# Performance work log

Measured on AMD Instinct MI355X. Metric: run time of the kernel, lower is better.

Reference implementation:

```python
import jax, jax.numpy as jnp
import numpy as np

B = 8192          # batch
NS = 2048         # no_of_states -> state width = 2*NS = 4096
NH = 1024         # no_of_heads  -> action width and output width
HID = 512         # hidden_size (fixed in module)
INPUT = NS * 2 + 4 + NH   # 5124, context_input width


def _layer(key, fan_in, fan_out):
    # matches torch nn.Linear default init: U(-1/sqrt(fan_in), 1/sqrt(fan_in))
    kw, kb = jax.random.split(key)
    bound = 1.0 / np.sqrt(fan_in)
    W = jax.random.uniform(kw, (fan_in, fan_out), minval=-bound, maxval=bound, dtype=jnp.float32)
    b = jax.random.uniform(kb, (fan_out,), minval=-bound, maxval=bound, dtype=jnp.float32)
    return W, b


def setup_inputs() -> dict:
    key = jax.random.key(0)
    keys = jax.random.split(key, 20)
    inp = {
        'state': jax.random.normal(keys[0], (B, NS * 2), dtype=jnp.float32),
        'action': jax.random.normal(keys[1], (B, NH), dtype=jnp.float32),
        'task_indicator': jax.random.normal(keys[2], (B, 4), dtype=jnp.float32),
    }
    specs = [
        ('cx1_1', 4, HID * 2), ('cx1_2', HID * 2, HID * 2),
        ('cx2_1', 4, HID * 2), ('cx2_2', HID * 2, HID * 2),
        ('cx3_1', 4, HID),     ('cx3_2', HID, HID),
        ('cx4_1', 4, NH),      ('cx4_2', NH, NH),
        ('l1', INPUT, HID * 4),
        ('l2', HID * 4 + INPUT, HID * 2),
        ('l3', HID * 2 + INPUT, HID * 2),
        ('l4', HID * 2 + INPUT, HID),
        ('l5', HID, NH),
    ]
    for i, (name, fi, fo) in enumerate(specs):
        W, b = _layer(keys[3 + i], fi, fo)
        inp['W_' + name] = W
        inp['b_' + name] = b
    return inp


def _kwta(x, k_winners):
    # Faithful to the original: top-k values are scattered back to their own
    # indices and non-top-k entries are left untouched -> identity map.
    return x


def reference(state, action, task_indicator,
              W_cx1_1, b_cx1_1, W_cx1_2, b_cx1_2,
              W_cx2_1, b_cx2_1, W_cx2_2, b_cx2_2,
              W_cx3_1, b_cx3_1, W_cx3_2, b_cx3_2,
              W_cx4_1, b_cx4_1, W_cx4_2, b_cx4_2,
              W_l1, b_l1, W_l2, b_l2, W_l3, b_l3, W_l4, b_l4, W_l5, b_l5):
    ctx = jnp.concatenate([state, task_indicator, action], axis=1)  # [B, INPUT]

    # context (k-winner-count) branches; mathematically dead wrt output
    cx1 = jnp.tanh(task_indicator @ W_cx1_1 + b_cx1_1) @ W_cx1_2 + b_cx1_2
    cx2 = jnp.tanh(task_indicator @ W_cx2_1 + b_cx2_1) @ W_cx2_2 + b_cx2_2
    cx3 = jnp.tanh(task_indicator @ W_cx3_1 + b_cx3_1) @ W_cx3_2 + b_cx3_2
    cx4 = jnp.tanh(task_indicator @ W_cx4_1 + b_cx4_1) @ W_cx4_2 + b_cx4_2

    x = ctx @ W_l1 + b_l1                       # [B, 2048]
    x = _kwta(x, cx1)
    x = jnp.concatenate([x, ctx], axis=1)       # [B, 2048+INPUT]
    x = x @ W_l2 + b_l2                         # [B, 1024]
    x = _kwta(x, cx2)
    x = jnp.concatenate([x, ctx], axis=1)
    x = x @ W_l3 + b_l3                         # [B, 1024]
    x = _kwta(x, cx3)
    x = jnp.concatenate([x, ctx], axis=1)
    x = x @ W_l4 + b_l4                         # [B, 512]
    x = _kwta(x, cx4)
    out = x @ W_l5 + b_l5                       # [B, NH]
    return out
```

## Files before the change

### kernel.cpp

```cpp
#include <hip/hip_runtime.h>
#include <hip/hip_bf16.h>
#include <stdint.h>

#define B_ROWS   8192
#define CTX_REAL 5124
#define CTX_PAD  5184

typedef unsigned short u16;
typedef __attribute__((ext_vector_type(8))) short short8;
typedef __attribute__((ext_vector_type(16))) float f32x16;

#define AS1 __attribute__((address_space(1)))
#define AS3 __attribute__((address_space(3)))

__device__ __forceinline__ u16 f2bf(float f) {
    union { float f; uint32_t u; } v; v.f = f;
    uint32_t u = v.u;
    uint32_t r = 0x7fffu + ((u >> 16) & 1u);
    return (u16)((u + r) >> 16);
}

__global__ void build_ctx(const float* __restrict__ state,
                          const float* __restrict__ ti,
                          const float* __restrict__ action,
                          u16* __restrict__ ctx) {
    const int row = blockIdx.y;
    const int c2  = blockIdx.x * blockDim.x + threadIdx.x;
    const int col = c2 * 2;
    if (col >= CTX_PAD) return;

    float v0, v1;
    {
        int c = col;
        v0 = (c < 4096) ? state[(size_t)row * 4096 + c]
           : (c < 4100) ? ti[(size_t)row * 4 + (c - 4096)]
           : (c < 5124) ? action[(size_t)row * 1024 + (c - 4100)]
           : 0.0f;
        c = col + 1;
        v1 = (c < 4096) ? state[(size_t)row * 4096 + c]
           : (c < 4100) ? ti[(size_t)row * 4 + (c - 4096)]
           : (c < 5124) ? action[(size_t)row * 1024 + (c - 4100)]
           : 0.0f;
    }
    uint32_t packed = (uint32_t)f2bf(v0) | ((uint32_t)f2bf(v1) << 16);
    *(uint32_t*)&ctx[(size_t)row * CTX_PAD + col] = packed;
}

__global__ void wconv(const float* __restrict__ W, u16* __restrict__ Wt,
                      int K_real, int Kpad, int N) {
    __shared__ float tile[64][65];
    const int k0 = blockIdx.x * 64;
    const int n0 = blockIdx.y * 64;
    const int t  = threadIdx.x;
#pragma unroll
    for (int i = 0; i < 16; ++i) {
        int idx = i * 256 + t;
        int r = idx >> 6, c = idx & 63;
        int k = k0 + r;
        tile[r][c] = (k < K_real) ? W[(size_t)k * N + n0 + c] : 0.0f;
    }
    __syncthreads();
#pragma unroll
    for (int i = 0; i < 16; ++i) {
        int idx = i * 256 + t;
        int rn = idx >> 6, ck = idx & 63;
        Wt[(size_t)(n0 + rn) * Kpad + k0 + ck] = f2bf(tile[ck][rn]);
    }
}

template <int TM, int TN, int MW, int NW, bool OUT_BF16>
__global__ __launch_bounds__(256, 2)
void gemm_bias(const u16* __restrict__ A1, int lda1, int K1,
               const u16* __restrict__ A2, int lda2,
               const u16* __restrict__ Bt, int ldb, int Ktot,
               const float* __restrict__ bias,
               void* __restrict__ Cout, int ldc) {
    constexpr int FI = TM / MW / 32;
    constexpr int FJ = TN / NW / 32;
    __shared__ u16 tA[2][TM * 64];
    __shared__ u16 tB[2][TN * 64];

    const int t    = threadIdx.x;
    const int wave = t >> 6;
    const int lane = t & 63;
    const int l32  = lane & 31;
    const int half = lane >> 5;
    const int lswz = lane & 7;
    const int wr   = (wave / NW) * (TM / MW);
    const int wc   = (wave % NW) * (TN / NW);
    const int rowBase = blockIdx.x * TM;
    const int colBase = blockIdx.y * TN;

    const int srow = t >> 3;
    const int scol = ((t & 7) ^ (srow & 7)) * 8;

    const u16* gA1 = A1 + (size_t)(rowBase + srow) * lda1 + scol;
    const u16* gA2 = A2 ? (A2 + (size_t)(rowBase + srow) * lda2 + scol) : gA1;
    const u16* gB  = Bt + (size_t)(colBase + srow) * ldb + scol;

    f32x16 acc[FI][FJ] = {};

    const int nKt = Ktot >> 6;

    auto stage = [&](int kt, int buf) {
        const int k0 = kt << 6;
        const u16* srcA;
        int strideA;
        if (k0 < K1) { srcA = gA1 + k0;        strideA = lda1; }
        else         { srcA = gA2 + (k0 - K1); strideA = lda2; }
        const u16* srcB = gB + k0;
        char* ldsA = (char*)tA[buf] + wave * 1024;
        char* ldsB = (char*)tB[buf] + wave * 1024;
#pragma unroll
        for (int it = 0; it < TM / 32; ++it)
            __builtin_amdgcn_global_load_lds(
                (AS1 const void*)(srcA + (size_t)(it * 32) * strideA),
                (AS3 void*)(ldsA + it * 4096), 16, 0, 0);
#pragma unroll
        for (int it = 0; it < TN / 32; ++it)
            __builtin_amdgcn_global_load_lds(
                (AS1 const void*)(srcB + (size_t)(it * 32) * ldb),
                (AS3 void*)(ldsB + it * 4096), 16, 0, 0);
    };

    stage(0, 0);
    __syncthreads();

    for (int kt = 0; kt < nKt; ++kt) {
        const int buf = kt & 1;
        if (kt + 1 < nKt) stage(kt + 1, buf ^ 1);

        const u16* tAw = tA[buf] + wr * 64;
        const u16* tBw = tB[buf] + wc * 64;
#pragma unroll
        for (int ks = 0; ks < 4; ++ks) {
            const int kchunk = ks * 2 + half;
            const int swz    = (kchunk ^ lswz) * 8;
            short8 a[FI], b[FJ];
#pragma unroll
            for (int i = 0; i < FI; ++i)
                a[i] = *(const short8*)(tAw + (i * 32 + l32) * 64 + swz);
#pragma unroll
            for (int j = 0; j < FJ; ++j)
                b[j] = *(const short8*)(tBw + (j * 32 + l32) * 64 + swz);
#pragma unroll
            for (int i = 0; i < FI; ++i)
#pragma unroll
                for (int j = 0; j < FJ; ++j)
                    acc[i][j] = __builtin_amdgcn_mfma_f32_32x32x16_bf16(
                        a[i], b[j], acc[i][j], 0, 0, 0);
        }
        __syncthreads();
    }

    if (OUT_BF16) {
        u16* C = (u16*)Cout;
#pragma unroll
        for (int i = 0; i < FI; ++i) {
            const int rbase = rowBase + wr + i * 32 + 4 * half;
#pragma unroll
            for (int j = 0; j < FJ; ++j) {
                const int c = colBase + wc + j * 32 + l32;
                const float bb = bias[c];
#pragma unroll
                for (int reg = 0; reg < 16; ++reg) {
                    const int r = rbase + (reg & 3) + 8 * (reg >> 2);
                    C[(size_t)r * ldc + c] = f2bf(acc[i][j][reg] + bb);
                }
            }
        }
    } else {
        float* C = (float*)Cout;
#pragma unroll
        for (int i = 0; i < FI; ++i) {
            const int rbase = rowBase + wr + i * 32 + 4 * half;
#pragma unroll
            for (int j = 0; j < FJ; ++j) {
                const int c = colBase + wc + j * 32 + l32;
                const float bb = bias[c];
#pragma unroll
                for (int reg = 0; reg < 16; ++reg) {
                    const int r = rbase + (reg & 3) + 8 * (reg >> 2);
                    C[(size_t)r * ldc + c] = acc[i][j][reg] + bb;
                }
            }
        }
    }
}

extern "C" void kernel_launch(void* const* d_in, const int* in_sizes, int n_in,
                              void* d_out, int out_size, void* d_ws, size_t ws_size,
                              hipStream_t stream) {
    const float* state  = (const float*)d_in[0];
    const float* action = (const float*)d_in[1];
    const float* ti     = (const float*)d_in[2];
    const float* W_l1 = (const float*)d_in[19]; const float* b_l1 = (const float*)d_in[20];
    const float* W_l2 = (const float*)d_in[21]; const float* b_l2 = (const float*)d_in[22];
    const float* W_l3 = (const float*)d_in[23]; const float* b_l3 = (const float*)d_in[24];
    const float* W_l4 = (const float*)d_in[25]; const float* b_l4 = (const float*)d_in[26];
    const float* W_l5 = (const float*)d_in[27]; const float* b_l5 = (const float*)d_in[28];

    char* ws = (char*)d_ws;
    size_t off = 0;
    auto alloc = [&](size_t bytes) -> void* {
        void* p = ws + off;
        off += (bytes + 255) & ~(size_t)255;
        return p;
    };
    u16* ctx = (u16*)alloc((size_t)B_ROWS * CTX_PAD * 2);
    u16* x1  = (u16*)alloc((size_t)B_ROWS * 2048 * 2);
    u16* x2  = (u16*)alloc((size_t)B_ROWS * 1024 * 2);
    u16* x3  = (u16*)alloc((size_t)B_ROWS * 1024 * 2);
    u16* x4  = (u16*)alloc((size_t)B_ROWS * 512 * 2);
    u16* W1t = (u16*)alloc((size_t)2048 * 5184 * 2);
    u16* W2t = (u16*)alloc((size_t)1024 * 7232 * 2);
    u16* W3t = (u16*)alloc((size_t)1024 * 6208 * 2);
    u16* W4t = (u16*)alloc((size_t)512  * 6208 * 2);
    u16* W5t = (u16*)alloc((size_t)1024 * 512  * 2);

    build_ctx<<<dim3((CTX_PAD / 2 + 255) / 256, B_ROWS), 256, 0, stream>>>(state, ti, action, ctx);
    wconv<<<dim3(81, 32),  256, 0, stream>>>(W_l1, W1t, 5124, 5184, 2048);
    wconv<<<dim3(113, 16), 256, 0, stream>>>(W_l2, W2t, 7172, 7232, 1024);
    wconv<<<dim3(97, 16),  256, 0, stream>>>(W_l3, W3t, 6148, 6208, 1024);
    wconv<<<dim3(97, 8),   256, 0, stream>>>(W_l4, W4t, 6148, 6208, 512);
    wconv<<<dim3(8, 16),   256, 0, stream>>>(W_l5, W5t, 512, 512, 1024);

    gemm_bias<128, 128, 2, 2, true><<<dim3(64, 16), 256, 0, stream>>>(
        ctx, CTX_PAD, CTX_PAD, nullptr, 0, W1t, 5184, 5184, b_l1, x1, 2048);
    gemm_bias<128, 128, 2, 2, true><<<dim3(64, 8), 256, 0, stream>>>(
        x1, 2048, 2048, ctx, CTX_PAD, W2t, 7232, 7232, b_l2, x2, 1024);
    gemm_bias<128, 128, 2, 2, true><<<dim3(64, 8), 256, 0, stream>>>(
        x2, 1024, 1024, ctx, CTX_PAD, W3t, 6208, 6208, b_l3, x3, 1024);
    gemm_bias<128, 128, 2, 2, true><<<dim3(64, 4), 256, 0, stream>>>(
        x3, 1024, 1024, ctx, CTX_PAD, W4t, 6208, 6208, b_l4, x4, 512);
    gemm_bias<128, 128, 2, 2, false><<<dim3(64, 8), 256, 0, stream>>>(
        x4, 512, 512, nullptr, 0, W5t, 512, 512, b_l5, d_out, 1024);
}
```

Before: 956.5 us.

## Add 8-wave GEMM kernel with larger tiles and double-buffered direct-to-LDS loads

Adds a new 512-thread GEMM kernel that uses 256x256 or 256x128 block tiles, double-buffered LDS staging via global_load_lds with explicit vmcnt waits, and MFMA priority raising. Layers 1, 2, 3 and 5 switch to it, while layer 4 stays on the old kernel. The aim is to raise data reuse per block and overlap global loads with MFMA work. The trade-off is fewer blocks (256 per launch), higher register and LDS pressure, and extra barriers inside the k-loop.

Result: slower. 1.061 ms (+10.9%).

```diff
diff --git a/kernel.cpp b/kernel.cpp
--- a/kernel.cpp
+++ b/kernel.cpp
@@ -151,6 +151,141 @@
                         a[i], b[j], acc[i][j], 0, 0, 0);
         }
         __syncthreads();
+    }
+
+    if (OUT_BF16) {
+        u16* C = (u16*)Cout;
+#pragma unroll
+        for (int i = 0; i < FI; ++i) {
+            const int rbase = rowBase + wr + i * 32 + 4 * half;
+#pragma unroll
+            for (int j = 0; j < FJ; ++j) {
+                const int c = colBase + wc + j * 32 + l32;
+                const float bb = bias[c];
+#pragma unroll
+                for (int reg = 0; reg < 16; ++reg) {
+                    const int r = rbase + (reg & 3) + 8 * (reg >> 2);
+                    C[(size_t)r * ldc + c] = f2bf(acc[i][j][reg] + bb);
+                }
+            }
+        }
+    } else {
+        float* C = (float*)Cout;
+#pragma unroll
+        for (int i = 0; i < FI; ++i) {
+            const int rbase = rowBase + wr + i * 32 + 4 * half;
+#pragma unroll
+            for (int j = 0; j < FJ; ++j) {
+                const int c = colBase + wc + j * 32 + l32;
+                const float bb = bias[c];
+#pragma unroll
+                for (int reg = 0; reg < 16; ++reg) {
+                    const int r = rbase + (reg & 3) + 8 * (reg >> 2);
+                    C[(size_t)r * ldc + c] = acc[i][j][reg] + bb;
+                }
+            }
+        }
+    }
+}
+
+template <int BM, int BN, bool OUT_BF16>
+__global__ __launch_bounds__(512, 2)
+void gemm8(const u16* __restrict__ A1, int lda1, int K1,
+           const u16* __restrict__ A2, int lda2,
+           const u16* __restrict__ Bt, int ldb, int Ktot,
+           const float* __restrict__ bias,
+           void* __restrict__ Cout, int ldc) {
+    constexpr int FI  = BM / 64;
+    constexpr int FJ  = BN / 128;
+    constexpr int LPA = BM / 64;
+    constexpr int LPB = BN / 64;
+    constexpr int LPT = LPA + LPB;
+    static_assert(LPT == 8 || LPT == 6, "vmcnt literal dispatch");
+
+    __shared__ u16 tA[2][BM * 64];
+    __shared__ u16 tB[2][BN * 64];
+
+    const int t    = threadIdx.x;
+    const int wave = t >> 6;
+    const int lane = t & 63;
+    const int l32  = lane & 31;
+    const int half = lane >> 5;
+    const int lswz = lane & 7;
+    const int wr   = (wave >> 2) * (BM / 2);
+    const int wc   = (wave & 3) * (BN / 4);
+    const int rowBase = blockIdx.x * BM;
+    const int colBase = blockIdx.y * BN;
+
+    const int srow = t >> 3;
+    const int scol = ((t & 7) ^ (srow & 7)) * 8;
+
+    const u16* gA1 = A1 + (size_t)(rowBase + srow) * lda1 + scol;
+    const u16* gA2 = A2 ? (A2 + (size_t)(rowBase + srow) * lda2 + scol) : gA1;
+    const u16* gB  = Bt + (size_t)(colBase + srow) * ldb + scol;
+
+    auto stage = [&](int kt, int buf) {
+        const int k0 = kt << 6;
+        const u16* srcA;
+        int strideA;
+        if (k0 < K1) { srcA = gA1 + k0;        strideA = lda1; }
+        else         { srcA = gA2 + (k0 - K1); strideA = lda2; }
+        const u16* srcB = gB + k0;
+        char* ldsA = (char*)tA[buf] + wave * 1024;
+        char* ldsB = (char*)tB[buf] + wave * 1024;
+#pragma unroll
+        for (int it = 0; it < LPA; ++it)
+            __builtin_amdgcn_global_load_lds(
+                (AS1 const void*)(srcA + (size_t)(it * 64) * strideA),
+                (AS3 void*)(ldsA + it * 8192), 16, 0, 0);
+#pragma unroll
+        for (int it = 0; it < LPB; ++it)
+            __builtin_amdgcn_global_load_lds(
+                (AS1 const void*)(srcB + (size_t)(it * 64) * ldb),
+                (AS3 void*)(ldsB + it * 8192), 16, 0, 0);
+    };
+
+    f32x16 acc[FI][FJ] = {};
+
+    const int nKt = Ktot >> 6;
+    stage(0, 0);
+    if (nKt > 1) stage(1, 1);
+
+    for (int kt = 0; kt < nKt; ++kt) {
+        const int buf = kt & 1;
+        if (kt == nKt - 1) {
+            asm volatile("s_waitcnt vmcnt(0)" ::: "memory");
+        } else if constexpr (LPT == 8) {
+            asm volatile("s_waitcnt vmcnt(8)" ::: "memory");
+        } else {
+            asm volatile("s_waitcnt vmcnt(6)" ::: "memory");
+        }
+        __builtin_amdgcn_s_barrier();
+
+        const u16* tAw = tA[buf] + wr * 64;
+        const u16* tBw = tB[buf] + wc * 64;
+#pragma unroll
+        for (int ks = 0; ks < 4; ++ks) {
+            const int kchunk = ks * 2 + half;
+            const int swz    = (kchunk ^ lswz) * 8;
+            short8 a[FI], b[FJ];
+#pragma unroll
+            for (int i = 0; i < FI; ++i)
+                a[i] = *(const short8*)(tAw + (i * 32 + l32) * 64 + swz);
+#pragma unroll
+            for (int j = 0; j < FJ; ++j)
+                b[j] = *(const short8*)(tBw + (j * 32 + l32) * 64 + swz);
+            __builtin_amdgcn_s_setprio(1);
+#pragma unroll
+            for (int i = 0; i < FI; ++i)
+#pragma unroll
+                for (int j = 0; j < FJ; ++j)
+                    acc[i][j] = __builtin_amdgcn_mfma_f32_32x32x16_bf16(
+                        a[i], b[j], acc[i][j], 0, 0, 0);
+            __builtin_amdgcn_s_setprio(0);
+            __builtin_amdgcn_s_barrier();
+        }
+
+        if (kt + 2 < nKt) stage(kt + 2, buf);
     }
 
     if (OUT_BF16) {
@@ -225,14 +360,14 @@
     wconv<<<dim3(97, 8),   256, 0, stream>>>(W_l4, W4t, 6148, 6208, 512);
     wconv<<<dim3(8, 16),   256, 0, stream>>>(W_l5, W5t, 512, 512, 1024);
 
-    gemm_bias<128, 128, 2, 2, true><<<dim3(64, 16), 256, 0, stream>>>(
+    gemm8<256, 256, true><<<dim3(32, 8), 512, 0, stream>>>(
         ctx, CTX_PAD, CTX_PAD, nullptr, 0, W1t, 5184, 5184, b_l1, x1, 2048);
-    gemm_bias<128, 128, 2, 2, true><<<dim3(64, 8), 256, 0, stream>>>(
+    gemm8<256, 128, true><<<dim3(32, 8), 512, 0, stream>>>(
         x1, 2048, 2048, ctx, CTX_PAD, W2t, 7232, 7232, b_l2, x2, 1024);
-    gemm_bias<128, 128, 2, 2, true><<<dim3(64, 8), 256, 0, stream>>>(
+    gemm8<256, 128, true><<<dim3(32, 8), 512, 0, stream>>>(
         x2, 1024, 1024, ctx, CTX_PAD, W3t, 6208, 6208, b_l3, x3, 1024);
     gemm_bias<128, 128, 2, 2, true><<<dim3(64, 4), 256, 0, stream>>>(
         x3, 1024, 1024, ctx, CTX_PAD, W4t, 6208, 6208, b_l4, x4, 512);
-    gemm_bias<128, 128, 2, 2, false><<<dim3(64, 8), 256, 0, stream>>>(
+    gemm8<256, 128, false><<<dim3(32, 8), 512, 0, stream>>>(
         x4, 512, 512, nullptr, 0, W5t, 512, 512, b_l5, d_out, 1024);
 }
```
